# Kernel optimization log

Hardware: AMD Instinct MI355X
Metric: run time of the kernel (lower is better)

Reference implementation:

```python
import jax, jax.numpy as jnp
import numpy as np

C = 1024
N_HEADS = 16
HEAD_DIM = C // N_HEADS
D_FF = 4 * C
EPS = 1e-5


def setup_inputs() -> dict:
    key = jax.random.key(0)
    ks = jax.random.split(key, 6)
    B, T = 4, 2048
    x = jax.random.normal(ks[0], (B, T, C), dtype=jnp.float32)
    w_qkv = jax.random.normal(ks[1], (C, 3 * C), dtype=jnp.float32) * (C ** -0.5)
    w_proj = jax.random.normal(ks[2], (C, C), dtype=jnp.float32) * (C ** -0.5)
    w1 = jax.random.normal(ks[3], (C, D_FF), dtype=jnp.float32) * (C ** -0.5)
    b1 = jnp.zeros((D_FF,), dtype=jnp.float32)
    w2 = jax.random.normal(ks[4], (D_FF, C), dtype=jnp.float32) * (D_FF ** -0.5)
    b2 = jnp.zeros((C,), dtype=jnp.float32)
    ln1_g = jnp.ones((C,), dtype=jnp.float32)
    ln1_b = jnp.zeros((C,), dtype=jnp.float32)
    ln2_g = jnp.ones((C,), dtype=jnp.float32)
    ln2_b = jnp.zeros((C,), dtype=jnp.float32)
    return {"x": x, "ln1_g": ln1_g, "ln1_b": ln1_b, "ln2_g": ln2_g,
            "ln2_b": ln2_b, "w_qkv": w_qkv, "w_proj": w_proj,
            "w1": w1, "b1": b1, "w2": w2, "b2": b2}


def _layernorm(x, g, b):
    mu = jnp.mean(x, axis=-1, keepdims=True)
    var = jnp.mean(jnp.square(x - mu), axis=-1, keepdims=True)
    return (x - mu) * jax.lax.rsqrt(var + EPS) * g + b


def _attention(x, w_qkv, w_proj):
    B, T, Cdim = x.shape
    qkv = x @ w_qkv                                   # [B,T,3C]
    q, k, v = jnp.split(qkv, 3, axis=-1)
    # [B,T,C] -> [B,H,T,D]
    def heads(t):
        return t.reshape(B, T, N_HEADS, HEAD_DIM).transpose(0, 2, 1, 3)
    q, k, v = heads(q), heads(k), heads(v)
    scale = HEAD_DIM ** -0.5
    scores = jnp.einsum('bhqd,bhkd->bhqk', q, k) * scale  # [B,H,T,T]
    attn = jax.nn.softmax(scores, axis=-1)
    out = jnp.einsum('bhqk,bhkd->bhqd', attn, v)          # [B,H,T,D]
    out = out.transpose(0, 2, 1, 3).reshape(B, T, Cdim)
    return out @ w_proj


def reference(x, ln1_g, ln1_b, ln2_g, ln2_b, w_qkv, w_proj, w1, b1, w2, b2):
    x = x + _attention(_layernorm(x, ln1_g, ln1_b), w_qkv, w_proj)
    h = _layernorm(x, ln2_g, ln2_b)
    # exact (erf) GELU matches torch.nn.GELU default
    h = jax.nn.gelu(h @ w1 + b1, approximate=False) @ w2 + b2
    return x + h
```

## Files before the change

kernel.cpp:

```cpp
#include <hip/hip_runtime.h>
#include <hip/hip_bf16.h>
#include <math.h>

typedef __attribute__((ext_vector_type(8))) short bf16x8;
typedef __attribute__((ext_vector_type(4))) float f32x4;
typedef unsigned short ushort_t;

__device__ __forceinline__ ushort_t f2bf(float f) {
    union { float f; unsigned u; } v; v.f = f;
    unsigned r = v.u + 0x7FFF + ((v.u >> 16) & 1);
    return (ushort_t)(r >> 16);
}

__device__ __forceinline__ unsigned pack2bf(float a, float b) {
    union { float f; unsigned u; } x, y; x.f = a; y.f = b;
    return __builtin_amdgcn_perm(y.u + 0x8000u, x.u + 0x8000u, 0x07060302u);
}

__device__ __forceinline__ unsigned cvtpk2bf(float a, float b) {
    unsigned r;
    asm("v_cvt_pk_bf16_f32 %0, %1, %2" : "=v"(r) : "v"(a), "v"(b));
    return r;
}

__device__ __forceinline__ void gl2lds(const void* g, void* l) {
    __builtin_amdgcn_global_load_lds(
        (const __attribute__((address_space(1))) void*)g,
        (__attribute__((address_space(3))) void*)l, 16, 0, 0);
}

__device__ __forceinline__ float fast_gelu(float tt) {
    float t2 = tt * tt;
    float arg = tt * fmaf(0.07135481283f, t2, 1.595769122f);
    float e = __builtin_amdgcn_exp2f(arg * -1.442695041f);
    return tt * __builtin_amdgcn_rcpf(1.0f + e);
}

__global__ __launch_bounds__(256)
void tcast_all(const float* __restrict__ wqkv, const float* __restrict__ wproj,
               const float* __restrict__ w1, const float* __restrict__ w2,
               ushort_t* __restrict__ wqkvT, ushort_t* __restrict__ wprojT,
               ushort_t* __restrict__ w1T, ushort_t* __restrict__ w2T,
               float qscale) {
    __shared__ float tile[32][33];
    int id = blockIdx.x;
    const float* in; ushort_t* out; int R, Cc, gx, scale_n;
    if (id < 3072)      { in = wqkv;  out = wqkvT;  R = 1024; Cc = 3072; gx = 96;  scale_n = 1024; }
    else if (id < 4096) { id -= 3072; in = wproj; out = wprojT; R = 1024; Cc = 1024; gx = 32; scale_n = 0; }
    else if (id < 8192) { id -= 4096; in = w1;    out = w1T;    R = 1024; Cc = 4096; gx = 128; scale_n = 0; }
    else                { id -= 8192; in = w2;    out = w2T;    R = 4096; Cc = 1024; gx = 32; scale_n = 0; }
    int bc = (id % gx) * 32, br = (id / gx) * 32;
    int tx = threadIdx.x, ty = threadIdx.y;
    #pragma unroll
    for (int i = 0; i < 32; i += 8)
        tile[ty + i][tx] = in[(size_t)(br + ty + i) * Cc + bc + tx];
    __syncthreads();
    #pragma unroll
    for (int i = 0; i < 32; i += 8) {
        int n = bc + ty + i;
        float v = tile[tx][ty + i];
        if (n < scale_n) v *= qscale;
        out[(size_t)n * R + br + tx] = f2bf(v);
    }
}

__global__ __launch_bounds__(256)
void ln_kernel(const float* __restrict__ x, const float* __restrict__ g,
               const float* __restrict__ b, ushort_t* __restrict__ out) {
    const int row = blockIdx.x;
    const int t = threadIdx.x;
    const float4 xv = ((const float4*)(x + (size_t)row * 1024))[t];
    float s  = xv.x + xv.y + xv.z + xv.w;
    float ss = xv.x*xv.x + xv.y*xv.y + xv.z*xv.z + xv.w*xv.w;
    #pragma unroll
    for (int off = 32; off > 0; off >>= 1) {
        s  += __shfl_xor(s, off);
        ss += __shfl_xor(ss, off);
    }
    __shared__ float red[8];
    int wave = t >> 6, lane = t & 63;
    if (lane == 0) { red[wave] = s; red[4 + wave] = ss; }
    __syncthreads();
    s  = red[0] + red[1] + red[2] + red[3];
    ss = red[4] + red[5] + red[6] + red[7];
    float mu  = s * (1.0f / 1024.0f);
    float var = ss * (1.0f / 1024.0f) - mu * mu;
    float rstd = rsqrtf(var + 1e-5f);
    float4 gv = ((const float4*)g)[t];
    float4 bv = ((const float4*)b)[t];
    ushort4 o;
    o.x = f2bf((xv.x - mu) * rstd * gv.x + bv.x);
    o.y = f2bf((xv.y - mu) * rstd * gv.y + bv.y);
    o.z = f2bf((xv.z - mu) * rstd * gv.z + bv.z);
    o.w = f2bf((xv.w - mu) * rstd * gv.w + bv.w);
    ((ushort4*)(out + (size_t)row * 1024))[t] = o;
}

template<int MODE, int K, int N>
__global__ __launch_bounds__(256)
void gemm_bt(const ushort_t* __restrict__ A, const ushort_t* __restrict__ Bt,
             void* __restrict__ Cout, const float* __restrict__ bias,
             const float* __restrict__ res, ushort_t* __restrict__ vTout) {
    constexpr int BK = 64;
    __shared__ __align__(16) ushort_t As[128 * 64];
    __shared__ __align__(16) ushort_t Bs[128 * 64];
    const int tid = threadIdx.x;
    const int wave = tid >> 6, lane = tid & 63;
    const int quad = lane >> 4, l16 = lane & 15;
    const int m0 = blockIdx.y * 128, n0 = blockIdx.x * 128;
    const int wm = (wave >> 1) * 64, wn = (wave & 1) * 64;

    const int r0 = tid >> 3, pc = tid & 7;
    const int lc = pc ^ (r0 & 7);
    const ushort_t* aSrc = A  + (size_t)(m0 + r0) * K + lc * 8;
    const ushort_t* bSrc = Bt + (size_t)(n0 + r0) * K + lc * 8;
    char* aDst = (char*)As + wave * 1024;
    char* bDst = (char*)Bs + wave * 1024;
    const int swz = l16 & 7;

    f32x4 acc[4][4] = {};

    for (int k0 = 0; k0 < K; k0 += BK) {
        __syncthreads();
        #pragma unroll
        for (int c = 0; c < 4; ++c) {
            gl2lds(aSrc + (size_t)c * 32 * K + k0, aDst + c * 4096);
            gl2lds(bSrc + (size_t)c * 32 * K + k0, bDst + c * 4096);
        }
        __syncthreads();
        #pragma unroll
        for (int ks = 0; ks < 2; ++ks) {
            const int cko = ((ks * 4 + quad) ^ swz) * 8;
            bf16x8 af[4], bfr[4];
            #pragma unroll
            for (int i = 0; i < 4; ++i)
                af[i] = *(const bf16x8*)(&As[(wm + i * 16 + l16) * 64 + cko]);
            #pragma unroll
            for (int j = 0; j < 4; ++j)
                bfr[j] = *(const bf16x8*)(&Bs[(wn + j * 16 + l16) * 64 + cko]);
            #pragma unroll
            for (int i = 0; i < 4; ++i)
                #pragma unroll
                for (int j = 0; j < 4; ++j)
                    acc[i][j] = __builtin_amdgcn_mfma_f32_16x16x32_bf16(
                        af[i], bfr[j], acc[i][j], 0, 0, 0);
        }
    }

    if constexpr (MODE == 0) {
        if (vTout && n0 >= 2048) {
            #pragma unroll
            for (int i = 0; i < 4; ++i) {
                int m = m0 + wm + i * 16 + quad * 4;
                int bb = m >> 11, t = m & 2047;
                #pragma unroll
                for (int j = 0; j < 4; ++j) {
                    int nn = n0 - 2048 + wn + j * 16 + l16;
                    int h = nn >> 6, d = nn & 63;
                    uint2 pk;
                    pk.x = pack2bf(acc[i][j][0], acc[i][j][1]);
                    pk.y = pack2bf(acc[i][j][2], acc[i][j][3]);
                    *(uint2*)(vTout + ((size_t)(bb * 16 + h) * 64 + d) * 2048 + t) = pk;
                }
            }
            return;
        }
    }
    float bj[4];
    if constexpr (MODE == 2 || MODE == 3) {
        #pragma unroll
        for (int j = 0; j < 4; ++j) bj[j] = bias[n0 + wn + j * 16 + l16];
    }
    #pragma unroll
    for (int i = 0; i < 4; ++i) {
        #pragma unroll
        for (int j = 0; j < 4; ++j) {
            #pragma unroll
            for (int r = 0; r < 4; ++r) {
                int m = m0 + wm + i * 16 + quad * 4 + r;
                int n = n0 + wn + j * 16 + l16;
                size_t idx = (size_t)m * N + n;
                float v = acc[i][j][r];
                if constexpr (MODE == 0) {
                    ((ushort_t*)Cout)[idx] = f2bf(v);
                } else if constexpr (MODE == 1) {
                    ((float*)Cout)[idx] = v + res[idx];
                } else if constexpr (MODE == 2) {
                    ((ushort_t*)Cout)[idx] = f2bf(fast_gelu(v + bj[j]));
                } else {
                    ((float*)Cout)[idx] = v + bj[j] + res[idx];
                }
            }
        }
    }
}

__global__ __launch_bounds__(256)
void attn_kernel(const ushort_t* __restrict__ qkv, const ushort_t* __restrict__ vT,
                 ushort_t* __restrict__ out) {
    constexpr int T = 2048, C3 = 3072, BQ = 128;
    __shared__ __align__(16) ushort_t Ks[2][64 * 64];
    __shared__ __align__(16) ushort_t Vs[2][64 * 64];
    const int bh = blockIdx.x, b = bh >> 4, h = bh & 15;
    const int qt = blockIdx.y;
    const int tid = threadIdx.x, wave = tid >> 6, lane = tid & 63;
    const int quad = lane >> 4, l16 = lane & 15;
    const int swz = l16 & 7;

    bf16x8 qf[2][2];
    {
        const ushort_t* Qg = qkv + ((size_t)b * T + qt * BQ + wave * 32) * C3 + h * 64;
        #pragma unroll
        for (int i = 0; i < 2; ++i)
            #pragma unroll
            for (int ks = 0; ks < 2; ++ks)
                qf[i][ks] = *(const bf16x8*)(Qg + (size_t)(i * 16 + l16) * C3 + ks * 32 + quad * 8);
    }
    bf16x8 onesf;
    #pragma unroll
    for (int e = 0; e < 8; ++e) onesf[e] = (short)0x3F80;

    const int r0 = tid >> 3, pc = tid & 7;
    const int lc = pc ^ (r0 & 7);
    const ushort_t* KgB = qkv + (size_t)b * T * C3 + 1024 + h * 64 + (size_t)r0 * C3 + lc * 8;
    const ushort_t* VgB = vT + (size_t)bh * 64 * T + (size_t)r0 * T + lc * 8;
    char* kDst0 = (char*)&Ks[0][0] + wave * 1024;
    char* vDst0 = (char*)&Vs[0][0] + wave * 1024;

    f32x4 o_acc[2][4] = {};
    f32x4 l_acc[2] = {};

    #pragma unroll
    for (int c = 0; c < 2; ++c) {
        gl2lds(KgB + (size_t)c * 32 * C3, kDst0 + c * 4096);
        gl2lds(VgB + (size_t)c * 32 * T,  vDst0 + c * 4096);
    }

    for (int kt = 0; kt < T / 64; ++kt) {
        const int cur = kt & 1;
        __syncthreads();
        if (kt + 1 < T / 64) {
            const int nb = (cur ^ 1) * 8192;
            #pragma unroll
            for (int c = 0; c < 2; ++c) {
                gl2lds(KgB + ((size_t)(kt + 1) * 64 + c * 32) * C3, kDst0 + nb + c * 4096);
                gl2lds(VgB + (size_t)c * 32 * T + (kt + 1) * 64,    vDst0 + nb + c * 4096);
            }
        }
        const ushort_t* Kc = &Ks[cur][0];
        const ushort_t* Vc = &Vs[cur][0];

        f32x4 s[2][4] = {};
        #pragma unroll
        for (int ks = 0; ks < 2; ++ks) {
            const int cko = ((ks * 4 + quad) ^ swz) * 8;
            bf16x8 kf[4];
            #pragma unroll
            for (int j = 0; j < 4; ++j)
                kf[j] = *(const bf16x8*)(&Kc[(j * 16 + l16) * 64 + cko]);
            #pragma unroll
            for (int i = 0; i < 2; ++i)
                #pragma unroll
                for (int j = 0; j < 4; ++j)
                    s[i][j] = __builtin_amdgcn_mfma_f32_16x16x32_bf16(
                        kf[j], qf[i][ks], s[i][j], 0, 0, 0);
        }

        bf16x8 pf[2][2];
        #pragma unroll
        for (int i = 0; i < 2; ++i) {
            unsigned u[4][2];
            #pragma unroll
            for (int j = 0; j < 4; ++j) {
                float p0 = __builtin_amdgcn_exp2f(s[i][j][0]);
                float p1 = __builtin_amdgcn_exp2f(s[i][j][1]);
                float p2 = __builtin_amdgcn_exp2f(s[i][j][2]);
                float p3 = __builtin_amdgcn_exp2f(s[i][j][3]);
                u[j][0] = cvtpk2bf(p0, p1);
                u[j][1] = cvtpk2bf(p2, p3);
            }
            #pragma unroll
            for (int ks2 = 0; ks2 < 2; ++ks2) {
                unsigned d0 = u[2 * ks2][0], d2 = u[2 * ks2 + 1][0];
                asm("v_permlane32_swap_b32 %0, %1\n\t"
                    "v_permlane16_swap_b32 %0, %1" : "+v"(d0), "+v"(d2));
                unsigned d1 = u[2 * ks2][1], d3 = u[2 * ks2 + 1][1];
                asm("v_permlane32_swap_b32 %0, %1\n\t"
                    "v_permlane16_swap_b32 %0, %1" : "+v"(d1), "+v"(d3));
                union { unsigned d[4]; bf16x8 v; } fr;
                fr.d[0] = d0; fr.d[1] = d1; fr.d[2] = d2; fr.d[3] = d3;
                pf[i][ks2] = fr.v;
            }
        }

        #pragma unroll
        for (int ks2 = 0; ks2 < 2; ++ks2) {
            const int cko = ((ks2 * 4 + quad) ^ swz) * 8;
            bf16x8 vf[4];
            #pragma unroll
            for (int j = 0; j < 4; ++j)
                vf[j] = *(const bf16x8*)(&Vc[(j * 16 + l16) * 64 + cko]);
            #pragma unroll
            for (int i = 0; i < 2; ++i) {
                #pragma unroll
                for (int j = 0; j < 4; ++j)
                    o_acc[i][j] = __builtin_amdgcn_mfma_f32_16x16x32_bf16(
                        pf[i][ks2], vf[j], o_acc[i][j], 0, 0, 0);
                l_acc[i] = __builtin_amdgcn_mfma_f32_16x16x32_bf16(
                    pf[i][ks2], onesf, l_acc[i], 0, 0, 0);
            }
        }
    }

    #pragma unroll
    for (int i = 0; i < 2; ++i) {
        #pragma unroll
        for (int r = 0; r < 4; ++r) {
            float inv = 1.0f / l_acc[i][r];
            int row = qt * BQ + wave * 32 + i * 16 + quad * 4 + r;
            size_t orow = ((size_t)b * T + row) * 1024 + h * 64;
            #pragma unroll
            for (int j = 0; j < 4; ++j)
                out[orow + j * 16 + l16] = f2bf(o_acc[i][j][r] * inv);
        }
    }
}

extern "C" void kernel_launch(void* const* d_in, const int* in_sizes, int n_in,
                              void* d_out, int out_size, void* d_ws, size_t ws_size,
                              hipStream_t stream) {
    const float* x     = (const float*)d_in[0];
    const float* ln1g  = (const float*)d_in[1];
    const float* ln1b  = (const float*)d_in[2];
    const float* ln2g  = (const float*)d_in[3];
    const float* ln2b  = (const float*)d_in[4];
    const float* wqkv  = (const float*)d_in[5];
    const float* wproj = (const float*)d_in[6];
    const float* w1    = (const float*)d_in[7];
    const float* b1    = (const float*)d_in[8];
    const float* w2    = (const float*)d_in[9];
    const float* b2    = (const float*)d_in[10];
    float* out = (float*)d_out;

    const size_t MT = 8192;
    ushort_t* wqkvT  = (ushort_t*)d_ws;
    ushort_t* wprojT = wqkvT  + (size_t)3072 * 1024;
    ushort_t* w1T    = wprojT + (size_t)1024 * 1024;
    ushort_t* w2T    = w1T    + (size_t)4096 * 1024;
    ushort_t* xn     = w2T    + (size_t)1024 * 4096;
    ushort_t* qkvb   = xn     + MT * 1024;
    ushort_t* attnb  = qkvb   + MT * 3072;
    float*    x2     = (float*)(attnb + MT * 1024);
    ushort_t* xn2    = (ushort_t*)(x2 + MT * 1024);
    ushort_t* h1     = xn;
    ushort_t* vT     = (ushort_t*)x2;

    dim3 blk256(256);
    dim3 tblk(32, 8);
    const float qscale = 0.125f * 1.4426950408889634f;

    tcast_all<<<dim3(12288), tblk, 0, stream>>>(wqkv, wproj, w1, w2,
                                                wqkvT, wprojT, w1T, w2T, qscale);

    ln_kernel<<<dim3(8192), blk256, 0, stream>>>(x, ln1g, ln1b, xn);
    gemm_bt<0, 1024, 3072><<<dim3(24, 64), blk256, 0, stream>>>(xn, wqkvT, qkvb, nullptr, nullptr, vT);
    attn_kernel<<<dim3(64, 16), blk256, 0, stream>>>(qkvb, vT, attnb);
    gemm_bt<1, 1024, 1024><<<dim3(8, 64), blk256, 0, stream>>>(attnb, wprojT, x2, nullptr, x, nullptr);
    ln_kernel<<<dim3(8192), blk256, 0, stream>>>(x2, ln2g, ln2b, xn2);
    gemm_bt<2, 1024, 4096><<<dim3(32, 64), blk256, 0, stream>>>(xn2, w1T, h1, b1, nullptr, nullptr);
    gemm_bt<3, 4096, 1024><<<dim3(8, 64), blk256, 0, stream>>>(h1, w2T, out, b2, x2, nullptr);
}
```

Before: 493.1 us.

## Restructure attention inner loop per query sub-tile and raise MFMA wave priority

The attention inner loop now computes scores, exp and PV for each 16-row query sub-tile in turn, instead of computing all scores first and then all PV products. This lowers live score registers and lets the exp work of one sub-tile overlap the MFMAs of the other. s_setprio brackets around the MFMA groups are meant to let waves issuing matrix ops win the scheduler. The cost is that K and V fragments are now loaded from LDS twice per tile, once per sub-tile, which adds LDS traffic.

New measurement: 503.7 us. 2.1% more time.

```diff
diff --git a/kernel.cpp b/kernel.cpp
--- a/kernel.cpp
+++ b/kernel.cpp
@@ -250,35 +250,35 @@
         const ushort_t* Kc = &Ks[cur][0];
         const ushort_t* Vc = &Vs[cur][0];
 
-        f32x4 s[2][4] = {};
-        #pragma unroll
-        for (int ks = 0; ks < 2; ++ks) {
-            const int cko = ((ks * 4 + quad) ^ swz) * 8;
-            bf16x8 kf[4];
-            #pragma unroll
-            for (int j = 0; j < 4; ++j)
-                kf[j] = *(const bf16x8*)(&Kc[(j * 16 + l16) * 64 + cko]);
-            #pragma unroll
-            for (int i = 0; i < 2; ++i)
-                #pragma unroll
-                for (int j = 0; j < 4; ++j)
-                    s[i][j] = __builtin_amdgcn_mfma_f32_16x16x32_bf16(
-                        kf[j], qf[i][ks], s[i][j], 0, 0, 0);
-        }
-
-        bf16x8 pf[2][2];
         #pragma unroll
         for (int i = 0; i < 2; ++i) {
+            f32x4 s1[4] = {};
+            #pragma unroll
+            for (int ks = 0; ks < 2; ++ks) {
+                const int cko = ((ks * 4 + quad) ^ swz) * 8;
+                bf16x8 kf[4];
+                #pragma unroll
+                for (int j = 0; j < 4; ++j)
+                    kf[j] = *(const bf16x8*)(&Kc[(j * 16 + l16) * 64 + cko]);
+                __builtin_amdgcn_s_setprio(1);
+                #pragma unroll
+                for (int j = 0; j < 4; ++j)
+                    s1[j] = __builtin_amdgcn_mfma_f32_16x16x32_bf16(
+                        kf[j], qf[i][ks], s1[j], 0, 0, 0);
+                __builtin_amdgcn_s_setprio(0);
+            }
+
             unsigned u[4][2];
             #pragma unroll
             for (int j = 0; j < 4; ++j) {
-                float p0 = __builtin_amdgcn_exp2f(s[i][j][0]);
-                float p1 = __builtin_amdgcn_exp2f(s[i][j][1]);
-                float p2 = __builtin_amdgcn_exp2f(s[i][j][2]);
-                float p3 = __builtin_amdgcn_exp2f(s[i][j][3]);
+                float p0 = __builtin_amdgcn_exp2f(s1[j][0]);
+                float p1 = __builtin_amdgcn_exp2f(s1[j][1]);
+                float p2 = __builtin_amdgcn_exp2f(s1[j][2]);
+                float p3 = __builtin_amdgcn_exp2f(s1[j][3]);
                 u[j][0] = cvtpk2bf(p0, p1);
                 u[j][1] = cvtpk2bf(p2, p3);
             }
+            bf16x8 pfi[2];
             #pragma unroll
             for (int ks2 = 0; ks2 < 2; ++ks2) {
                 unsigned d0 = u[2 * ks2][0], d2 = u[2 * ks2 + 1][0];
@@ -289,25 +289,24 @@
                     "v_permlane16_swap_b32 %0, %1" : "+v"(d1), "+v"(d3));
                 union { unsigned d[4]; bf16x8 v; } fr;
                 fr.d[0] = d0; fr.d[1] = d1; fr.d[2] = d2; fr.d[3] = d3;
-                pf[i][ks2] = fr.v;
-            }
-        }
-
-        #pragma unroll
-        for (int ks2 = 0; ks2 < 2; ++ks2) {
-            const int cko = ((ks2 * 4 + quad) ^ swz) * 8;
-            bf16x8 vf[4];
-            #pragma unroll
-            for (int j = 0; j < 4; ++j)
-                vf[j] = *(const bf16x8*)(&Vc[(j * 16 + l16) * 64 + cko]);
-            #pragma unroll
-            for (int i = 0; i < 2; ++i) {
+                pfi[ks2] = fr.v;
+            }
+
+            #pragma unroll
+            for (int ks2 = 0; ks2 < 2; ++ks2) {
+                const int cko = ((ks2 * 4 + quad) ^ swz) * 8;
+                bf16x8 vf[4];
+                #pragma unroll
+                for (int j = 0; j < 4; ++j)
+                    vf[j] = *(const bf16x8*)(&Vc[(j * 16 + l16) * 64 + cko]);
+                __builtin_amdgcn_s_setprio(1);
                 #pragma unroll
                 for (int j = 0; j < 4; ++j)
                     o_acc[i][j] = __builtin_amdgcn_mfma_f32_16x16x32_bf16(
-                        pf[i][ks2], vf[j], o_acc[i][j], 0, 0, 0);
+                        pfi[ks2], vf[j], o_acc[i][j], 0, 0, 0);
                 l_acc[i] = __builtin_amdgcn_mfma_f32_16x16x32_bf16(
-                    pf[i][ks2], onesf, l_acc[i], 0, 0, 0);
+                    pfi[ks2], onesf, l_acc[i], 0, 0, 0);
+                __builtin_amdgcn_s_setprio(0);
             }
         }
     }
```

## Triple-buffer GEMM loads with 256x128 tiles, 512 threads and XCD-aware block remap

Applied to the files above, without the earlier changes.

Replaces the single-buffered GEMM with a three-stage LDS ring, prefetching two K-tiles ahead using vmcnt waits, so global-to-LDS loads overlap MFMA work. Block tiles grow to 256x128 with 8 waves, block IDs are remapped across the 8 XCDs for cache locality, and MFMA sections are wrapped with s_setprio. The larger LDS footprint (about 144KB) limits occupancy, and the hand-set vmcnt counts must match the number of issued loads.

Result: slower. 537.9 us (+9.1%).

```diff
diff --git a/kernel.cpp b/kernel.cpp
--- a/kernel.cpp
+++ b/kernel.cpp
@@ -97,62 +97,88 @@
 }
 
 template<int MODE, int K, int N>
-__global__ __launch_bounds__(256)
-void gemm_bt(const ushort_t* __restrict__ A, const ushort_t* __restrict__ Bt,
-             void* __restrict__ Cout, const float* __restrict__ bias,
-             const float* __restrict__ res, ushort_t* __restrict__ vTout) {
+__global__ __launch_bounds__(512, 2)
+void gemm3b(const ushort_t* __restrict__ A, const ushort_t* __restrict__ Bt,
+            void* __restrict__ Cout, const float* __restrict__ bias,
+            const float* __restrict__ res, ushort_t* __restrict__ vTout) {
     constexpr int BK = 64;
-    __shared__ __align__(16) ushort_t As[128 * 64];
-    __shared__ __align__(16) ushort_t Bs[128 * 64];
+    constexpr int NT = K / BK;
+    __shared__ __align__(16) ushort_t As[3][256 * 64];
+    __shared__ __align__(16) ushort_t Bs[3][128 * 64];
     const int tid = threadIdx.x;
     const int wave = tid >> 6, lane = tid & 63;
     const int quad = lane >> 4, l16 = lane & 15;
-    const int m0 = blockIdx.y * 128, n0 = blockIdx.x * 128;
+    const int nwg = gridDim.x * gridDim.y;
+    int id = blockIdx.y * gridDim.x + blockIdx.x;
+    id = (id & 7) * (nwg >> 3) + (id >> 3);
+    const int m0 = (id / gridDim.x) * 256, n0 = (id % gridDim.x) * 128;
     const int wm = (wave >> 1) * 64, wn = (wave & 1) * 64;
 
     const int r0 = tid >> 3, pc = tid & 7;
     const int lc = pc ^ (r0 & 7);
     const ushort_t* aSrc = A  + (size_t)(m0 + r0) * K + lc * 8;
     const ushort_t* bSrc = Bt + (size_t)(n0 + r0) * K + lc * 8;
-    char* aDst = (char*)As + wave * 1024;
-    char* bDst = (char*)Bs + wave * 1024;
     const int swz = l16 & 7;
 
     f32x4 acc[4][4] = {};
 
-    for (int k0 = 0; k0 < K; k0 += BK) {
-        __syncthreads();
-        #pragma unroll
-        for (int c = 0; c < 4; ++c) {
-            gl2lds(aSrc + (size_t)c * 32 * K + k0, aDst + c * 4096);
-            gl2lds(bSrc + (size_t)c * 32 * K + k0, bDst + c * 4096);
-        }
-        __syncthreads();
+    #define STAGE3(tt, bb) do { \
+        const size_t ko = (size_t)(tt) * BK; \
+        char* aD = (char*)&As[bb][0] + wave * 1024; \
+        char* bD = (char*)&Bs[bb][0] + wave * 1024; \
+        _Pragma("unroll") \
+        for (int c = 0; c < 4; ++c) \
+            gl2lds(aSrc + (size_t)c * 64 * K + ko, aD + c * 8192); \
+        _Pragma("unroll") \
+        for (int c = 0; c < 2; ++c) \
+            gl2lds(bSrc + (size_t)c * 64 * K + ko, bD + c * 8192); \
+    } while (0)
+
+    STAGE3(0, 0);
+    STAGE3(1, 1);
+
+    for (int t = 0; t < NT; ++t) {
+        const int cur = t % 3;
+        if (t + 2 < NT) {
+            STAGE3(t + 2, (t + 2) % 3);
+            asm volatile("s_waitcnt vmcnt(12)" ::: "memory");
+        } else if (t + 1 < NT) {
+            asm volatile("s_waitcnt vmcnt(6)" ::: "memory");
+        } else {
+            asm volatile("s_waitcnt vmcnt(0)" ::: "memory");
+        }
+        __builtin_amdgcn_s_barrier();
+        const ushort_t* Ac = &As[cur][0];
+        const ushort_t* Bc = &Bs[cur][0];
         #pragma unroll
         for (int ks = 0; ks < 2; ++ks) {
             const int cko = ((ks * 4 + quad) ^ swz) * 8;
             bf16x8 af[4], bfr[4];
             #pragma unroll
             for (int i = 0; i < 4; ++i)
-                af[i] = *(const bf16x8*)(&As[(wm + i * 16 + l16) * 64 + cko]);
+                af[i] = *(const bf16x8*)(&Ac[(wm + i * 16 + l16) * 64 + cko]);
             #pragma unroll
             for (int j = 0; j < 4; ++j)
-                bfr[j] = *(const bf16x8*)(&Bs[(wn + j * 16 + l16) * 64 + cko]);
+                bfr[j] = *(const bf16x8*)(&Bc[(wn + j * 16 + l16) * 64 + cko]);
+            __builtin_amdgcn_s_setprio(1);
             #pragma unroll
             for (int i = 0; i < 4; ++i)
                 #pragma unroll
                 for (int j = 0; j < 4; ++j)
                     acc[i][j] = __builtin_amdgcn_mfma_f32_16x16x32_bf16(
                         af[i], bfr[j], acc[i][j], 0, 0, 0);
-        }
-    }
+            __builtin_amdgcn_s_setprio(0);
+        }
+        __builtin_amdgcn_s_barrier();
+    }
+    #undef STAGE3
 
     if constexpr (MODE == 0) {
         if (vTout && n0 >= 2048) {
             #pragma unroll
             for (int i = 0; i < 4; ++i) {
                 int m = m0 + wm + i * 16 + quad * 4;
-                int bb = m >> 11, t = m & 2047;
+                int bb = m >> 11, tq = m & 2047;
                 #pragma unroll
                 for (int j = 0; j < 4; ++j) {
                     int nn = n0 - 2048 + wn + j * 16 + l16;
@@ -160,7 +186,7 @@
                     uint2 pk;
                     pk.x = pack2bf(acc[i][j][0], acc[i][j][1]);
                     pk.y = pack2bf(acc[i][j][2], acc[i][j][3]);
-                    *(uint2*)(vTout + ((size_t)(bb * 16 + h) * 64 + d) * 2048 + t) = pk;
+                    *(uint2*)(vTout + ((size_t)(bb * 16 + h) * 64 + d) * 2048 + tq) = pk;
                 }
             }
             return;
@@ -356,6 +382,7 @@
     ushort_t* vT     = (ushort_t*)x2;
 
     dim3 blk256(256);
+    dim3 blk512(512);
     dim3 tblk(32, 8);
     const float qscale = 0.125f * 1.4426950408889634f;
 
@@ -363,10 +390,10 @@
                                                 wqkvT, wprojT, w1T, w2T, qscale);
 
     ln_kernel<<<dim3(8192), blk256, 0, stream>>>(x, ln1g, ln1b, xn);
-    gemm_bt<0, 1024, 3072><<<dim3(24, 64), blk256, 0, stream>>>(xn, wqkvT, qkvb, nullptr, nullptr, vT);
+    gemm3b<0, 1024, 3072><<<dim3(24, 32), blk512, 0, stream>>>(xn, wqkvT, qkvb, nullptr, nullptr, vT);
     attn_kernel<<<dim3(64, 16), blk256, 0, stream>>>(qkvb, vT, attnb);
-    gemm_bt<1, 1024, 1024><<<dim3(8, 64), blk256, 0, stream>>>(attnb, wprojT, x2, nullptr, x, nullptr);
+    gemm3b<1, 1024, 1024><<<dim3(8, 32), blk512, 0, stream>>>(attnb, wprojT, x2, nullptr, x, nullptr);
     ln_kernel<<<dim3(8192), blk256, 0, stream>>>(x2, ln2g, ln2b, xn2);
-    gemm_bt<2, 1024, 4096><<<dim3(32, 64), blk256, 0, stream>>>(xn2, w1T, h1, b1, nullptr, nullptr);
-    gemm_bt<3, 4096, 1024><<<dim3(8, 64), blk256, 0, stream>>>(h1, w2T, out, b2, x2, nullptr);
-}
+    gemm3b<2, 1024, 4096><<<dim3(32, 32), blk512, 0, stream>>>(xn2, w1T, h1, b1, nullptr, nullptr);
+    gemm3b<3, 4096, 1024><<<dim3(8, 32), blk512, 0, stream>>>(h1, w2T, out, b2, x2, nullptr);
+}
```

## Replace GEMM with 8-wave 128x256 double-buffered pipelined kernel with block swizzle

Applied to the files above, without the earlier changes.

Replaces the single-buffered 4-wave 128x128 GEMM with an 8-wave 128x256 tile kernel that double-buffers A/B in LDS and interleaves global-to-LDS loads with MFMA phases under fine-grained barriers and waitcnts. It also remaps block IDs across XCDs so neighbouring tiles share L2, and raises MFMA priority during the compute phases. The aim is to hide global load latency and improve operand reuse. In exchange it uses more LDS and registers per block, and the hand-written pipeline is fragile if vmcnt counts or barrier placement are off.

Result: no change. 496.8 us (+0.8%).

```diff
diff --git a/kernel.cpp b/kernel.cpp
--- a/kernel.cpp
+++ b/kernel.cpp
@@ -97,62 +97,98 @@
 }
 
 template<int MODE, int K, int N>
-__global__ __launch_bounds__(256)
-void gemm_bt(const ushort_t* __restrict__ A, const ushort_t* __restrict__ Bt,
-             void* __restrict__ Cout, const float* __restrict__ bias,
-             const float* __restrict__ res, ushort_t* __restrict__ vTout) {
+__global__ __launch_bounds__(512, 2)
+void gemm8p(const ushort_t* __restrict__ A, const ushort_t* __restrict__ Bt,
+            void* __restrict__ Cout, const float* __restrict__ bias,
+            const float* __restrict__ res, ushort_t* __restrict__ vTout) {
     constexpr int BK = 64;
-    __shared__ __align__(16) ushort_t As[128 * 64];
-    __shared__ __align__(16) ushort_t Bs[128 * 64];
+    constexpr int NT = K / BK;
+    constexpr int ITERS = NT / 2;
+    __shared__ __align__(16) ushort_t As[2][128 * 64];
+    __shared__ __align__(16) ushort_t Bs[2][256 * 64];
     const int tid = threadIdx.x;
     const int wave = tid >> 6, lane = tid & 63;
     const int quad = lane >> 4, l16 = lane & 15;
-    const int m0 = blockIdx.y * 128, n0 = blockIdx.x * 128;
-    const int wm = (wave >> 1) * 64, wn = (wave & 1) * 64;
-
+    const int nwg = gridDim.x * gridDim.y;
+    int id = blockIdx.y * gridDim.x + blockIdx.x;
+    id = (id & 7) * (nwg >> 3) + (id >> 3);
+    const int gx = N / 256;
+    const int m0 = (id / gx) * 128, n0 = (id % gx) * 256;
+    const int wm = (wave >> 2) * 64, wn = (wave & 3) * 64;
     const int r0 = tid >> 3, pc = tid & 7;
     const int lc = pc ^ (r0 & 7);
     const ushort_t* aSrc = A  + (size_t)(m0 + r0) * K + lc * 8;
     const ushort_t* bSrc = Bt + (size_t)(n0 + r0) * K + lc * 8;
-    char* aDst = (char*)As + wave * 1024;
-    char* bDst = (char*)Bs + wave * 1024;
     const int swz = l16 & 7;
 
     f32x4 acc[4][4] = {};
-
-    for (int k0 = 0; k0 < K; k0 += BK) {
-        __syncthreads();
-        #pragma unroll
-        for (int c = 0; c < 4; ++c) {
-            gl2lds(aSrc + (size_t)c * 32 * K + k0, aDst + c * 4096);
-            gl2lds(bSrc + (size_t)c * 32 * K + k0, bDst + c * 4096);
-        }
-        __syncthreads();
-        #pragma unroll
-        for (int ks = 0; ks < 2; ++ks) {
-            const int cko = ((ks * 4 + quad) ^ swz) * 8;
-            bf16x8 af[4], bfr[4];
-            #pragma unroll
-            for (int i = 0; i < 4; ++i)
-                af[i] = *(const bf16x8*)(&As[(wm + i * 16 + l16) * 64 + cko]);
-            #pragma unroll
-            for (int j = 0; j < 4; ++j)
-                bfr[j] = *(const bf16x8*)(&Bs[(wn + j * 16 + l16) * 64 + cko]);
-            #pragma unroll
-            for (int i = 0; i < 4; ++i)
-                #pragma unroll
-                for (int j = 0; j < 4; ++j)
-                    acc[i][j] = __builtin_amdgcn_mfma_f32_16x16x32_bf16(
-                        af[i], bfr[j], acc[i][j], 0, 0, 0);
-        }
-    }
+    bf16x8 bfr[4][2], af[2][2];
+
+    #define STA(t, b, c) gl2lds(aSrc + (size_t)(t) * BK + (size_t)(c) * 64 * K, \
+                                (char*)&As[b][0] + (c) * 8192 + wave * 1024)
+    #define STB(t, b, c) gl2lds(bSrc + (size_t)(t) * BK + (size_t)(c) * 64 * K, \
+                                (char*)&Bs[b][0] + (c) * 8192 + wave * 1024)
+    #define LDB(buf) { _Pragma("unroll") for (int j = 0; j < 4; ++j) \
+        _Pragma("unroll") for (int ks = 0; ks < 2; ++ks) \
+            bfr[j][ks] = *(const bf16x8*)(&Bs[buf][(wn + j * 16 + l16) * 64 + ((ks * 4 + quad) ^ swz) * 8]); }
+    #define LDA2(buf, fb) { _Pragma("unroll") for (int f = 0; f < 2; ++f) \
+        _Pragma("unroll") for (int ks = 0; ks < 2; ++ks) \
+            af[f][ks] = *(const bf16x8*)(&As[buf][(wm + ((fb) + f) * 16 + l16) * 64 + ((ks * 4 + quad) ^ swz) * 8]); }
+    #define OPENBAR { __builtin_amdgcn_s_barrier(); \
+        asm volatile("s_waitcnt lgkmcnt(0)" ::: "memory"); \
+        __builtin_amdgcn_sched_barrier(0); }
+    #define MM(fb) { __builtin_amdgcn_s_setprio(1); \
+        _Pragma("unroll") for (int ks = 0; ks < 2; ++ks) \
+        _Pragma("unroll") for (int f = 0; f < 2; ++f) \
+        _Pragma("unroll") for (int j = 0; j < 4; ++j) \
+            acc[(fb) + f][j] = __builtin_amdgcn_mfma_f32_16x16x32_bf16( \
+                af[f][ks], bfr[j][ks], acc[(fb) + f][j], 0, 0, 0); \
+        __builtin_amdgcn_s_setprio(0); }
+
+    STA(0, 0, 0); STA(0, 0, 1);
+    STB(0, 0, 0); STB(0, 0, 1); STB(0, 0, 2); STB(0, 0, 3);
+    STB(1, 1, 0); STB(1, 1, 1); STB(1, 1, 2);
+    asm volatile("s_waitcnt vmcnt(3)" ::: "memory");
+    __builtin_amdgcn_s_barrier();
+
+    for (int i = 0; i < ITERS; ++i) {
+        const int e = 2 * i, o = 2 * i + 1;
+        const bool pre = (i + 1 < ITERS);
+        LDB(0); LDA2(0, 0);
+        STB(o, 1, 3); STA(o, 1, 0); STA(o, 1, 1);
+        OPENBAR; MM(0);
+        __builtin_amdgcn_s_barrier();
+        LDA2(0, 2);
+        if (pre) { STB(e + 2, 0, 0); STB(e + 2, 0, 1); STB(e + 2, 0, 2); }
+        OPENBAR; MM(2);
+        if (pre) asm volatile("s_waitcnt vmcnt(3)" ::: "memory");
+        else     asm volatile("s_waitcnt vmcnt(0)" ::: "memory");
+        __builtin_amdgcn_s_barrier();
+        LDB(1); LDA2(1, 0);
+        if (pre) { STB(e + 2, 0, 3); STA(e + 2, 0, 0); STA(e + 2, 0, 1); }
+        OPENBAR; MM(0);
+        __builtin_amdgcn_s_barrier();
+        LDA2(1, 2);
+        if (pre) { STB(o + 2, 1, 0); STB(o + 2, 1, 1); STB(o + 2, 1, 2); }
+        OPENBAR; MM(2);
+        if (pre) {
+            asm volatile("s_waitcnt vmcnt(3)" ::: "memory");
+            __builtin_amdgcn_s_barrier();
+        }
+    }
+    #undef STA
+    #undef STB
+    #undef LDB
+    #undef LDA2
+    #undef OPENBAR
+    #undef MM
 
     if constexpr (MODE == 0) {
         if (vTout && n0 >= 2048) {
             #pragma unroll
             for (int i = 0; i < 4; ++i) {
                 int m = m0 + wm + i * 16 + quad * 4;
-                int bb = m >> 11, t = m & 2047;
+                int bb = m >> 11, tq = m & 2047;
                 #pragma unroll
                 for (int j = 0; j < 4; ++j) {
                     int nn = n0 - 2048 + wn + j * 16 + l16;
@@ -160,7 +196,7 @@
                     uint2 pk;
                     pk.x = pack2bf(acc[i][j][0], acc[i][j][1]);
                     pk.y = pack2bf(acc[i][j][2], acc[i][j][3]);
-                    *(uint2*)(vTout + ((size_t)(bb * 16 + h) * 64 + d) * 2048 + t) = pk;
+                    *(uint2*)(vTout + ((size_t)(bb * 16 + h) * 64 + d) * 2048 + tq) = pk;
                 }
             }
             return;
@@ -356,6 +392,7 @@
     ushort_t* vT     = (ushort_t*)x2;
 
     dim3 blk256(256);
+    dim3 blk512(512);
     dim3 tblk(32, 8);
     const float qscale = 0.125f * 1.4426950408889634f;
 
@@ -363,10 +400,10 @@
                                                 wqkvT, wprojT, w1T, w2T, qscale);
 
     ln_kernel<<<dim3(8192), blk256, 0, stream>>>(x, ln1g, ln1b, xn);
-    gemm_bt<0, 1024, 3072><<<dim3(24, 64), blk256, 0, stream>>>(xn, wqkvT, qkvb, nullptr, nullptr, vT);
+    gemm8p<0, 1024, 3072><<<dim3(12, 64), blk512, 0, stream>>>(xn, wqkvT, qkvb, nullptr, nullptr, vT);
     attn_kernel<<<dim3(64, 16), blk256, 0, stream>>>(qkvb, vT, attnb);
-    gemm_bt<1, 1024, 1024><<<dim3(8, 64), blk256, 0, stream>>>(attnb, wprojT, x2, nullptr, x, nullptr);
+    gemm8p<1, 1024, 1024><<<dim3(4, 64), blk512, 0, stream>>>(attnb, wprojT, x2, nullptr, x, nullptr);
     ln_kernel<<<dim3(8192), blk256, 0, stream>>>(x2, ln2g, ln2b, xn2);
-    gemm_bt<2, 1024, 4096><<<dim3(32, 64), blk256, 0, stream>>>(xn2, w1T, h1, b1, nullptr, nullptr);
-    gemm_bt<3, 4096, 1024><<<dim3(8, 64), blk256, 0, stream>>>(h1, w2T, out, b2, x2, nullptr);
-}
+    gemm8p<2, 1024, 4096><<<dim3(16, 64), blk512, 0, stream>>>(xn2, w1T, h1, b1, nullptr, nullptr);
+    gemm8p<3, 4096, 1024><<<dim3(4, 64), blk512, 0, stream>>>(h1, w2T, out, b2, x2, nullptr);
+}
```
